# Performance work log

Measured on AMD Instinct MI355X. Metric: run time of the kernel, lower is better.

The kernel has to match this reference:

```python
import jax, jax.numpy as jnp
import numpy as np

B, S, D = 4, 2048, 1024
H = 16
DH = D // H  # 64
DFF = 4096
EPS = 1e-5


def _layer_norm(x, g, b):
    mu = jnp.mean(x, axis=-1, keepdims=True)
    var = jnp.mean((x - mu) ** 2, axis=-1, keepdims=True)
    return (x - mu) * jax.lax.rsqrt(var + EPS) * g + b


def _rope(x):
    # x: [B, S, H, DH]; same rotation for every head (module reuses one RoPE).
    inv_freq = 1.0 / (10000.0 ** (jnp.arange(0, DH, 2, dtype=jnp.float32) / DH))
    pos = jnp.arange(S, dtype=jnp.float32)
    freqs = pos[:, None] * inv_freq[None, :]            # [S, DH/2]
    cos = jnp.cos(freqs)[None, :, None, :]              # [1, S, 1, DH/2]
    sin = jnp.sin(freqs)[None, :, None, :]
    x_even = x[..., 0::2]
    x_odd = x[..., 1::2]
    r_even = x_even * cos - x_odd * sin
    r_odd = x_even * sin + x_odd * cos
    return jnp.stack([r_even, r_odd], axis=-1).reshape(x.shape)


def setup_inputs() -> dict:
    key = jax.random.key(0)
    ks = jax.random.split(key, 10)
    s_d = 1.0 / np.sqrt(D)
    s_f = 1.0 / np.sqrt(DFF)
    return {
        "x": jax.random.normal(ks[0], (B, S, D), jnp.float32),
        "Wq": jax.random.uniform(ks[1], (D, D), jnp.float32, -s_d, s_d),
        "bq": jnp.zeros((D,), jnp.float32),
        "Wk": jax.random.uniform(ks[2], (D, D), jnp.float32, -s_d, s_d),
        "bk": jnp.zeros((D,), jnp.float32),
        "Wv": jax.random.uniform(ks[3], (D, D), jnp.float32, -s_d, s_d),
        "bv": jnp.zeros((D,), jnp.float32),
        "Wo": jax.random.uniform(ks[4], (D, D), jnp.float32, -s_d, s_d),
        "bo": jnp.zeros((D,), jnp.float32),
        "W1": jax.random.uniform(ks[5], (DFF, D), jnp.float32, -s_d, s_d),
        "bf1": jnp.zeros((DFF,), jnp.float32),
        "W2": jax.random.uniform(ks[6], (D, DFF), jnp.float32, -s_f, s_f),
        "bf2": jnp.zeros((D,), jnp.float32),
        "g1": jnp.ones((D,), jnp.float32),
        "be1": jnp.zeros((D,), jnp.float32),
        "g2": jnp.ones((D,), jnp.float32),
        "be2": jnp.zeros((D,), jnp.float32),
    }


def reference(x, Wq, bq, Wk, bk, Wv, bv, Wo, bo, W1, bf1, W2, bf2, g1, be1, g2, be2):
    # Pre-LN self-attention block (dropout is identity at eval)
    residual = x
    h = _layer_norm(x, g1, be1)
    q = (h @ Wq.T + bq).reshape(B, S, H, DH)
    k = (h @ Wk.T + bk).reshape(B, S, H, DH)
    v = (h @ Wv.T + bv).reshape(B, S, H, DH)
    q = _rope(q)
    k = _rope(k)
    # scores: [B, H, Sq, Sk]
    scores = jnp.einsum("bqhd,bkhd->bhqk", q, k) / np.sqrt(DH)
    causal = jnp.tril(jnp.ones((S, S), dtype=bool))
    scores = jnp.where(causal[None, None], scores, -jnp.inf)
    attn = jax.nn.softmax(scores, axis=-1)
    out = jnp.einsum("bhqk,bkhd->bqhd", attn, v).reshape(B, S, D)
    out = out @ Wo.T + bo
    x = residual + out
    # FFN block
    residual = x
    h = _layer_norm(x, g2, be2)
    ff = jax.nn.relu(h @ W1.T + bf1) @ W2.T + bf2
    return residual + ff
```

## Files before the change

### kernel.cpp

```cpp
#include <hip/hip_runtime.h>

typedef __attribute__((ext_vector_type(8))) short bh8;
typedef __attribute__((ext_vector_type(4))) short sh4;
typedef __attribute__((ext_vector_type(4))) float f4;
typedef __attribute__((ext_vector_type(16))) float f16v;
typedef __attribute__((ext_vector_type(4))) unsigned int u4;

__device__ __forceinline__ unsigned short f2bf(float x) {
  unsigned int u = __float_as_uint(x);
  u += 0x7fffu + ((u >> 16) & 1u);
  return (unsigned short)(u >> 16);
}
__device__ __forceinline__ float bf2f(short x) {
  return __uint_as_float(((unsigned int)(unsigned short)x) << 16);
}
__device__ __forceinline__ unsigned cvtpk_bf16(float lo, float hi) {
  unsigned r;
  asm("v_cvt_pk_bf16_f32 %0, %1, %2" : "=v"(r) : "v"(lo), "v"(hi));
  return r;
}
__device__ __forceinline__ void gl_lds16(const short* g, short* l) {
  __builtin_amdgcn_global_load_lds(
      (const __attribute__((address_space(1))) unsigned int*)g,
      (__attribute__((address_space(3))) unsigned int*)l, 16, 0, 0);
}

#define VM2() asm volatile("s_waitcnt vmcnt(2)" ::: "memory")
#define VM0() asm volatile("s_waitcnt vmcnt(0)" ::: "memory")

__global__ __launch_bounds__(256)
void rope_table(float* __restrict__ ct, float* __restrict__ st) {
  const int idx = blockIdx.x * 256 + threadIdx.x;
  const int s = idx >> 5, j = idx & 31;
  const float invf = expf(-0.28782313662425574f * (float)j);
  const float f = (float)s * invf;
  ct[idx] = cosf(f);
  st[idx] = sinf(f);
}

__global__ __launch_bounds__(256)
void concat_bias(const float* __restrict__ bq, const float* __restrict__ bk,
                 const float* __restrict__ bv, float* __restrict__ bqkv) {
  const int i = blockIdx.x * 256 + threadIdx.x;
  bqkv[i] = (i < 1024) ? bq[i] : ((i < 2048) ? bk[i - 1024] : bv[i - 2048]);
}

__global__ __launch_bounds__(256)
void w2bf_all(const float* __restrict__ Wq, const float* __restrict__ Wk,
              const float* __restrict__ Wv, const float* __restrict__ Wo,
              const float* __restrict__ W1, const float* __restrict__ W2,
              short* __restrict__ wqkvb, short* __restrict__ wob,
              short* __restrict__ w1b, short* __restrict__ w2b) {
  const int which = blockIdx.y;
  const float* src; short* dst; int n;
  switch (which) {
    case 0: src = Wq; dst = wqkvb;                 n = 1 << 20; break;
    case 1: src = Wk; dst = wqkvb + (1 << 20);     n = 1 << 20; break;
    case 2: src = Wv; dst = wqkvb + (2 << 20);     n = 1 << 20; break;
    case 3: src = Wo; dst = wob;                   n = 1 << 20; break;
    case 4: src = W1; dst = w1b;                   n = 1 << 22; break;
    default: src = W2; dst = w2b;                  n = 1 << 22; break;
  }
  const int i = (blockIdx.x * 256 + threadIdx.x) * 4;
  if (i >= n) return;
  f4 v = *(const f4*)(src + i);
#pragma unroll
  for (int j = 0; j < 4; ++j) dst[i + j] = (short)f2bf(v[j]);
}

__global__ __launch_bounds__(256)
void layernorm_bf(const float* __restrict__ x, const float* __restrict__ g,
                  const float* __restrict__ be, short* __restrict__ out) {
  __shared__ float sb[4];
  const int row = blockIdx.x, t = threadIdx.x;
  const float* xr = x + (size_t)row * 1024;
  f4 v = *(const f4*)(xr + t * 4);
  float s = v[0] + v[1] + v[2] + v[3];
#pragma unroll
  for (int mk = 1; mk < 64; mk <<= 1) s += __shfl_xor(s, mk, 64);
  if ((t & 63) == 0) sb[t >> 6] = s;
  __syncthreads();
  const float mean = (sb[0] + sb[1] + sb[2] + sb[3]) * (1.0f / 1024.0f);
  __syncthreads();
  f4 d;
#pragma unroll
  for (int i = 0; i < 4; ++i) d[i] = v[i] - mean;
  float s2 = d[0] * d[0] + d[1] * d[1] + d[2] * d[2] + d[3] * d[3];
#pragma unroll
  for (int mk = 1; mk < 64; mk <<= 1) s2 += __shfl_xor(s2, mk, 64);
  if ((t & 63) == 0) sb[t >> 6] = s2;
  __syncthreads();
  const float var = (sb[0] + sb[1] + sb[2] + sb[3]) * (1.0f / 1024.0f);
  const float rstd = rsqrtf(var + 1e-5f);
  const f4 gg = *(const f4*)(g + t * 4);
  const f4 bb = *(const f4*)(be + t * 4);
#pragma unroll
  for (int i = 0; i < 4; ++i)
    out[(size_t)row * 1024 + t * 4 + i] = (short)f2bf(d[i] * rstd * gg[i] + bb[i]);
}

#define STG(dst, gbase, kt, half)                                              \
  {                                                                            \
    _Pragma("unroll") for (int cc = 0; cc < 2; ++cc) {                         \
      const int rr = (half) * 128 + cc * 64 + sr;                              \
      gl_lds16(gbase + (size_t)rr * K + (kt) * 64 + ssl * 8,                   \
               &dst[rr * 64 + (t & 7) * 8]);                                   \
    }                                                                          \
  }

#define PH64(bf, q, STAGE_STMT, VMSTMT)                                        \
  {                                                                            \
    if ((q) == 0) {                                                            \
      _Pragma("unroll") for (int ni = 0; ni < 2; ++ni)                         \
      _Pragma("unroll") for (int kk = 0; kk < 2; ++kk)                         \
        bfrag[ni][kk] = *(const bh8*)(&Bs[bf][(wn * 32 + ni * 16 + (lane & 15)) * 64 + (((lane >> 4) + kk * 4) ^ (lane & 7)) * 8]); \
    }                                                                          \
    _Pragma("unroll") for (int j = 0; j < 2; ++j)                              \
    _Pragma("unroll") for (int kk = 0; kk < 2; ++kk)                           \
      af[j][kk] = *(const bh8*)(&As[bf][(wm * 64 + (2 * (q) + j) * 16 + (lane & 15)) * 64 + (((lane >> 4) + kk * 4) ^ (lane & 7)) * 8]); \
    STAGE_STMT;                                                                \
    __builtin_amdgcn_s_barrier();                                              \
    asm volatile("s_waitcnt lgkmcnt(0)" ::: "memory");                         \
    __builtin_amdgcn_sched_barrier(0);                                         \
    __builtin_amdgcn_s_setprio(1);                                             \
    _Pragma("unroll") for (int j = 0; j < 2; ++j)                              \
    _Pragma("unroll") for (int ni = 0; ni < 2; ++ni)                           \
    _Pragma("unroll") for (int kk = 0; kk < 2; ++kk)                           \
      acc[2 * (q) + j][ni] = __builtin_amdgcn_mfma_f32_16x16x32_bf16(          \
          af[j][kk], bfrag[ni][kk], acc[2 * (q) + j][ni], 0, 0, 0);            \
    __builtin_amdgcn_s_setprio(0);                                             \
    VMSTMT;                                                                    \
    __builtin_amdgcn_s_barrier();                                              \
  }

template <int RELU, int RES, int OBF16, int QKVMODE>
__global__ __launch_bounds__(512, 4)
void gemm_bn128(const short* __restrict__ A, const short* __restrict__ Bw,
                const float* __restrict__ bias, const float* __restrict__ res,
                const float* __restrict__ ct, const float* __restrict__ st,
                short* __restrict__ Vt,
                short* __restrict__ Cb, float* __restrict__ Cf,
                int M, int N, int K) {
  __shared__ short As[2][128 * 64];
  __shared__ short Bs[2][128 * 64];
  const int t = threadIdx.x, lane = t & 63;
  const int w = t >> 6, wm = w >> 2, wn = w & 3;
  const int nwg = gridDim.x, cpx = nwg >> 3;
  int flat = blockIdx.x;
  flat = (flat & 7) * cpx + (flat >> 3);
  const int nbn = N >> 7;
  const int bn = flat % nbn, bm = flat / nbn;
  const short* Ab = A + (size_t)(bm * 128) * K;
  const short* Bb = Bw + (size_t)(bn * 128) * K;
  const int nkt = K >> 6;
  const int sr = t >> 3;
  const int ssl = (t & 7) ^ (sr & 7);
  f4 acc[4][2] = {};
  bh8 bfrag[2][2], af[2][2];

  STG(Bs[0], Bb, 0, 0); STG(As[0], Ab, 0, 0);
  STG(Bs[1], Bb, 1, 0);
  VM2();
  __builtin_amdgcn_s_barrier();

  for (int i2 = 0; i2 < nkt; i2 += 2) {
    const bool nf = (i2 + 2 < nkt);
    PH64(0, 0, STG(As[1], Ab, i2 + 1, 0), );
    PH64(0, 1, if (nf) STG(Bs[0], Bb, i2 + 2, 0),
         if (nf) { VM2(); } else { VM0(); });
    PH64(1, 0, if (nf) STG(As[0], Ab, i2 + 2, 0), );
    PH64(1, 1, if (nf) STG(Bs[1], Bb, i2 + 3, 0), if (nf) { VM2(); });
  }

  const int rb = bm * 128 + wm * 64 + ((lane >> 4) << 2);
  const int cb = bn * 128 + wn * 32 + (lane & 15);
  if (QKVMODE && bn >= 16) {
#pragma unroll
    for (int mi = 0; mi < 4; ++mi) {
#pragma unroll
      for (int ni = 0; ni < 2; ++ni) {
        const int c = cb + ni * 16;
        const float bi = bias[c];
        const int hh = (c - 2048) >> 6, dd = (c - 2048) & 63;
        const int r0 = rb + mi * 16;
        const int bb2 = r0 >> 11, ss = r0 & 2047;
        sh4 pk;
#pragma unroll
        for (int jr = 0; jr < 4; ++jr) pk[jr] = (short)f2bf(acc[mi][ni][jr] + bi);
        *(sh4*)(Vt + ((size_t)(bb2 * 16 + hh) * 64 + dd) * 2048 + ss) = pk;
      }
    }
  } else if (QKVMODE) {
    const bool evenc = (lane & 1) == 0;
#pragma unroll
    for (int mi = 0; mi < 4; ++mi) {
#pragma unroll
      for (int ni = 0; ni < 2; ++ni) {
        const int c = cb + ni * 16;
        const float bi = bias[c];
        const int j0 = (c & 63) >> 1;
#pragma unroll
        for (int jr = 0; jr < 4; ++jr) {
          const int r = rb + mi * 16 + jr;
          const int s = r & 2047;
          const float v = acc[mi][ni][jr] + bi;
          const float pv = __shfl_xor(v, 1, 64);
          const float cs = ct[s * 32 + j0], sn = st[s * 32 + j0];
          const float o = evenc ? (v * cs - pv * sn) : (pv * sn + v * cs);
          Cb[(size_t)r * N + c] = (short)f2bf(o);
        }
      }
    }
  } else {
#pragma unroll
    for (int mi = 0; mi < 4; ++mi) {
#pragma unroll
      for (int ni = 0; ni < 2; ++ni) {
        const int c = cb + ni * 16;
        const float bi = bias[c];
#pragma unroll
        for (int jr = 0; jr < 4; ++jr) {
          const int r = rb + mi * 16 + jr;
          float v = acc[mi][ni][jr] + bi;
          if (RES) v += res[(size_t)r * N + c];
          if (RELU) v = fmaxf(v, 0.f);
          if (OBF16) Cb[(size_t)r * N + c] = (short)f2bf(v);
          else       Cf[(size_t)r * N + c] = v;
        }
      }
    }
  }
}

__global__ __launch_bounds__(512, 4)
void flash_attn(const short* __restrict__ qkv, const short* __restrict__ vt,
                short* __restrict__ o) {
  __shared__ short lds[2 * 2 * 64 * 72];
  const int t = threadIdx.x, lane = t & 63, w = t >> 6;
  const int l31 = lane & 31, l5 = lane >> 5;
  const int id = blockIdx.x;
  const int half = id >> 8, j = id & 255;
  const int xcd = j & 7, y = j >> 3;
  const int bh = xcd * 8 + (y >> 2);
  const int pr = y & 3;
  const int qt = half ? pr : 7 - pr;
  const int b = bh >> 4, hh = bh & 15;
  const int r8 = t >> 3, c8 = (t & 7) * 8;
  const float NEG_INF = -__builtin_inff();

  const short* kbase = qkv + (size_t)b * 2048 * 3072 + 1024 + hh * 64;
  const short* vbase = vt + ((size_t)bh * 64 + r8) * 2048;
  const int wq0 = qt * 256 + w * 32;
  const int nt = 4 * qt + 4;

  bh8 qf[4];
  {
    const short* qrow = qkv + ((size_t)b * 2048 + wq0 + l31) * 3072 + hh * 64 + l5 * 8;
#pragma unroll
    for (int dk = 0; dk < 4; ++dk) qf[dk] = *(const bh8*)(qrow + dk * 16);
  }
  f16v o0 = {}, o1 = {};
  float mr = NEG_INF, lsum = 0.f;

  {
    bh8 rk = *(const bh8*)(kbase + (size_t)r8 * 3072 + c8);
    bh8 rv = *(const bh8*)(vbase + c8);
    *(bh8*)(&lds[r8 * 72 + c8]) = rk;
    *(bh8*)(&lds[4608 + r8 * 72 + c8]) = rv;
  }

  for (int kt = 0; kt < nt; ++kt) {
    __syncthreads();
    const int cur = kt & 1, nxt = cur ^ 1;
    bh8 rk, rv;
    const bool more = (kt + 1 < nt);
    if (more) {
      rk = *(const bh8*)(kbase + (size_t)((kt + 1) * 64 + r8) * 3072 + c8);
      rv = *(const bh8*)(vbase + (kt + 1) * 64 + c8);
    }
    const int kvb = kt * 64;
    if (kvb <= wq0 + 31) {
      const short* Kl = &lds[cur * 9216];
      const short* Vl = &lds[cur * 9216 + 4608];
      f16v s0 = {}, s1 = {};
#pragma unroll
      for (int dk = 0; dk < 4; ++dk) {
        bh8 ka0 = *(const bh8*)(&Kl[l31 * 72 + dk * 16 + l5 * 8]);
        bh8 ka1 = *(const bh8*)(&Kl[(32 + l31) * 72 + dk * 16 + l5 * 8]);
        s0 = __builtin_amdgcn_mfma_f32_32x32x16_bf16(ka0, qf[dk], s0, 0, 0, 0);
        s1 = __builtin_amdgcn_mfma_f32_32x32x16_bf16(ka1, qf[dk], s1, 0, 0, 0);
      }
      if (kvb + 63 > wq0) {
        const int qq = wq0 + l31;
        const int kvo = kvb + l5 * 4;
#pragma unroll
        for (int r = 0; r < 16; ++r) {
          const int kv0 = kvo + (r & 3) + 8 * (r >> 2);
          if (kv0 > qq) s0[r] = NEG_INF;
          if (kv0 + 32 > qq) s1[r] = NEG_INF;
        }
      }
      float mx = s0[0];
#pragma unroll
      for (int r = 1; r < 16; ++r) mx = fmaxf(mx, s0[r]);
#pragma unroll
      for (int r = 0; r < 16; ++r) mx = fmaxf(mx, s1[r]);
      mx = fmaxf(mx, __shfl_xor(mx, 32, 64));
      const bool keep = __all(mx <= mr + 8.0f);
      float mn, al;
      if (keep) { mn = mr; al = 1.0f; }
      else {
        mn = fmaxf(mr, mx);
        al = __expf((mr - mn) * 0.125f);
        mr = mn;
      }
      float rsA = 0.f, rsB = 0.f;
#pragma unroll
      for (int r = 0; r < 16; ++r) {
        const float p0 = __expf((s0[r] - mn) * 0.125f);
        const float p1 = __expf((s1[r] - mn) * 0.125f);
        s0[r] = p0; s1[r] = p1;
        rsA += p0; rsB += p1;
      }
      float rs = rsA + rsB;
      rs += __shfl_xor(rs, 32, 64);
      if (keep) {
        lsum += rs;
      } else {
        lsum = lsum * al + rs;
#pragma unroll
        for (int r = 0; r < 16; ++r) { o0[r] *= al; o1[r] *= al; }
      }
      float pp[32];
#pragma unroll
      for (int r = 0; r < 16; ++r) { pp[r] = s0[r]; pp[16 + r] = s1[r]; }
      const bool lo32 = (l5 == 0);
#pragma unroll
      for (int ks = 0; ks < 4; ++ks) {
        const int base = (ks >> 1) * 16 + (ks & 1) * 8;
        const unsigned e0 = cvtpk_bf16(pp[base + 0], pp[base + 1]);
        const unsigned e1 = cvtpk_bf16(pp[base + 2], pp[base + 3]);
        const unsigned q0 = cvtpk_bf16(pp[base + 4], pp[base + 5]);
        const unsigned q1 = cvtpk_bf16(pp[base + 6], pp[base + 7]);
        const unsigned sel0 = lo32 ? q0 : e0;
        const unsigned sel1 = lo32 ? q1 : e1;
        const unsigned rx0 = (unsigned)__shfl_xor((int)sel0, 32, 64);
        const unsigned rx1 = (unsigned)__shfl_xor((int)sel1, 32, 64);
        u4 frag;
        frag[0] = lo32 ? e0 : rx0;
        frag[1] = lo32 ? e1 : rx1;
        frag[2] = lo32 ? rx0 : q0;
        frag[3] = lo32 ? rx1 : q1;
        const bh8 pb = *(const bh8*)&frag;
        bh8 va0 = *(const bh8*)(&Vl[l31 * 72 + ks * 16 + l5 * 8]);
        bh8 va1 = *(const bh8*)(&Vl[(32 + l31) * 72 + ks * 16 + l5 * 8]);
        o0 = __builtin_amdgcn_mfma_f32_32x32x16_bf16(va0, pb, o0, 0, 0, 0);
        o1 = __builtin_amdgcn_mfma_f32_32x32x16_bf16(va1, pb, o1, 0, 0, 0);
      }
    }
    if (more) {
      *(bh8*)(&lds[nxt * 9216 + r8 * 72 + c8]) = rk;
      *(bh8*)(&lds[nxt * 9216 + 4608 + r8 * 72 + c8]) = rv;
    }
  }

  const float inv = 1.0f / lsum;
  __syncthreads();
  short* Ot = lds;
#pragma unroll
  for (int r = 0; r < 16; ++r) {
    const int d = (r & 3) + 8 * (r >> 2) + 4 * l5;
    Ot[(w * 32 + l31) * 72 + d]      = (short)f2bf(o0[r] * inv);
    Ot[(w * 32 + l31) * 72 + 32 + d] = (short)f2bf(o1[r] * inv);
  }
  __syncthreads();
  const int qrow = t >> 1, hf = t & 1;
  short* orow = o + ((size_t)b * 2048 + qt * 256 + qrow) * 1024 + hh * 64 + hf * 32;
#pragma unroll
  for (int i = 0; i < 4; ++i)
    *(bh8*)(orow + i * 8) = *(const bh8*)(&Ot[qrow * 72 + hf * 32 + i * 8]);
}

extern "C" void kernel_launch(void* const* d_in, const int* in_sizes, int n_in,
                              void* d_out, int out_size, void* d_ws, size_t ws_size,
                              hipStream_t stream) {
  const float* x   = (const float*)d_in[0];
  const float* Wq  = (const float*)d_in[1];
  const float* bq  = (const float*)d_in[2];
  const float* Wk  = (const float*)d_in[3];
  const float* bk  = (const float*)d_in[4];
  const float* Wv  = (const float*)d_in[5];
  const float* bv  = (const float*)d_in[6];
  const float* Wo  = (const float*)d_in[7];
  const float* bo  = (const float*)d_in[8];
  const float* W1  = (const float*)d_in[9];
  const float* bf1 = (const float*)d_in[10];
  const float* W2  = (const float*)d_in[11];
  const float* bf2 = (const float*)d_in[12];
  const float* g1  = (const float*)d_in[13];
  const float* be1 = (const float*)d_in[14];
  const float* g2  = (const float*)d_in[15];
  const float* be2 = (const float*)d_in[16];
  float* out = (float*)d_out;

  char* ws = (char*)d_ws;
  const size_t MB = 1u << 20;
  short* h_ob  = (short*)ws;
  short* qkv   = (short*)(ws + 16 * MB);
  short* f1    = (short*)(ws + 16 * MB);
  short* vtb   = (short*)(ws + 64 * MB);
  short* wqkvb = (short*)(ws + 80 * MB);
  short* wob   = (short*)(ws + 86 * MB);
  short* w1b   = (short*)(ws + 88 * MB);
  short* w2b   = (short*)(ws + 96 * MB);
  float* ct    = (float*)(ws + 104 * MB);
  float* st    = ct + 65536;
  float* bqkv  = st + 65536;
  float* x2    = out;

  rope_table<<<256, 256, 0, stream>>>(ct, st);
  concat_bias<<<12, 256, 0, stream>>>(bq, bk, bv, bqkv);
  w2bf_all<<<dim3(4096, 6), 256, 0, stream>>>(Wq, Wk, Wv, Wo, W1, W2,
                                              wqkvb, wob, w1b, w2b);

  layernorm_bf<<<8192, 256, 0, stream>>>(x, g1, be1, h_ob);

  gemm_bn128<0, 0, 1, 1><<<1536, 512, 0, stream>>>(h_ob, wqkvb, bqkv, nullptr,
                                                   ct, st, vtb, qkv, nullptr,
                                                   8192, 3072, 1024);

  flash_attn<<<512, 512, 0, stream>>>(qkv, vtb, h_ob);

  gemm_bn128<0, 1, 0, 0><<<512, 512, 0, stream>>>(h_ob, wob, bo, x,
                                                  nullptr, nullptr, nullptr,
                                                  nullptr, x2, 8192, 1024, 1024);

  layernorm_bf<<<8192, 256, 0, stream>>>(x2, g2, be2, h_ob);

  gemm_bn128<1, 0, 1, 0><<<2048, 512, 0, stream>>>(h_ob, w1b, bf1, nullptr,
                                                   nullptr, nullptr, nullptr,
                                                   f1, nullptr, 8192, 4096, 1024);

  gemm_bn128<0, 1, 0, 0><<<512, 512, 0, stream>>>(f1, w2b, bf2, x2,
                                                  nullptr, nullptr, nullptr,
                                                  nullptr, out, 8192, 1024, 4096);
}
```

Before: 360.1 us.

## Restructure GEMM to BK=32 triple-buffered LDS pipeline with higher occupancy

Replaces the double-buffered 64-wide K tile GEMM with a 32-wide K tile and a three-slot ring of LDS buffers, prefetching two tiles ahead. The LDS footprint drops from 64KB to 48KB and launch bounds rise from 4 to 6 waves/EU, aiming for more resident workgroups and better latency hiding. The swizzle changes to a 4-slot XOR pattern to match the narrower rows. In exchange there are twice as many barriers per unit of K work, fewer MFMAs per barrier, and tighter register limits.

Measured after the change: 380.7 us. 5.7% more time.

```diff
diff --git a/kernel.cpp b/kernel.cpp
--- a/kernel.cpp
+++ b/kernel.cpp
@@ -99,50 +99,39 @@
     out[(size_t)row * 1024 + t * 4 + i] = (short)f2bf(d[i] * rstd * gg[i] + bb[i]);
 }
 
-#define STG(dst, gbase, kt, half)                                              \
+#define STG32(dst, gbase, kt)                                                  \
+  gl_lds16(gbase + (size_t)sr32 * K + (kt) * 32 + ssl32 * 8, (dst) + t * 8);
+
+#define PH32(Ac, Bc, STAGE_STMT, VMSTMT)                                       \
   {                                                                            \
-    _Pragma("unroll") for (int cc = 0; cc < 2; ++cc) {                         \
-      const int rr = (half) * 128 + cc * 64 + sr;                              \
-      gl_lds16(gbase + (size_t)rr * K + (kt) * 64 + ssl * 8,                   \
-               &dst[rr * 64 + (t & 7) * 8]);                                   \
-    }                                                                          \
-  }
-
-#define PH64(bf, q, STAGE_STMT, VMSTMT)                                        \
-  {                                                                            \
-    if ((q) == 0) {                                                            \
-      _Pragma("unroll") for (int ni = 0; ni < 2; ++ni)                         \
-      _Pragma("unroll") for (int kk = 0; kk < 2; ++kk)                         \
-        bfrag[ni][kk] = *(const bh8*)(&Bs[bf][(wn * 32 + ni * 16 + (lane & 15)) * 64 + (((lane >> 4) + kk * 4) ^ (lane & 7)) * 8]); \
-    }                                                                          \
-    _Pragma("unroll") for (int j = 0; j < 2; ++j)                              \
-    _Pragma("unroll") for (int kk = 0; kk < 2; ++kk)                           \
-      af[j][kk] = *(const bh8*)(&As[bf][(wm * 64 + (2 * (q) + j) * 16 + (lane & 15)) * 64 + (((lane >> 4) + kk * 4) ^ (lane & 7)) * 8]); \
+    _Pragma("unroll") for (int j = 0; j < 4; ++j)                              \
+      af[j] = *(const bh8*)(&(Ac)[(wm * 64 + j * 16 + (lane & 15)) * 32 + rslot]); \
+    _Pragma("unroll") for (int ni = 0; ni < 2; ++ni)                           \
+      bfrag[ni] = *(const bh8*)(&(Bc)[(wn * 32 + ni * 16 + (lane & 15)) * 32 + rslot]); \
     STAGE_STMT;                                                                \
     __builtin_amdgcn_s_barrier();                                              \
     asm volatile("s_waitcnt lgkmcnt(0)" ::: "memory");                         \
     __builtin_amdgcn_sched_barrier(0);                                         \
     __builtin_amdgcn_s_setprio(1);                                             \
-    _Pragma("unroll") for (int j = 0; j < 2; ++j)                              \
+    _Pragma("unroll") for (int j = 0; j < 4; ++j)                              \
     _Pragma("unroll") for (int ni = 0; ni < 2; ++ni)                           \
-    _Pragma("unroll") for (int kk = 0; kk < 2; ++kk)                           \
-      acc[2 * (q) + j][ni] = __builtin_amdgcn_mfma_f32_16x16x32_bf16(          \
-          af[j][kk], bfrag[ni][kk], acc[2 * (q) + j][ni], 0, 0, 0);            \
+      acc[j][ni] = __builtin_amdgcn_mfma_f32_16x16x32_bf16(                    \
+          af[j], bfrag[ni], acc[j][ni], 0, 0, 0);                              \
     __builtin_amdgcn_s_setprio(0);                                             \
     VMSTMT;                                                                    \
     __builtin_amdgcn_s_barrier();                                              \
   }
 
 template <int RELU, int RES, int OBF16, int QKVMODE>
-__global__ __launch_bounds__(512, 4)
-void gemm_bn128(const short* __restrict__ A, const short* __restrict__ Bw,
-                const float* __restrict__ bias, const float* __restrict__ res,
-                const float* __restrict__ ct, const float* __restrict__ st,
-                short* __restrict__ Vt,
-                short* __restrict__ Cb, float* __restrict__ Cf,
-                int M, int N, int K) {
-  __shared__ short As[2][128 * 64];
-  __shared__ short Bs[2][128 * 64];
+__global__ __launch_bounds__(512, 6)
+void gemm_tb(const short* __restrict__ A, const short* __restrict__ Bw,
+             const float* __restrict__ bias, const float* __restrict__ res,
+             const float* __restrict__ ct, const float* __restrict__ st,
+             short* __restrict__ Vt,
+             short* __restrict__ Cb, float* __restrict__ Cf,
+             int M, int N, int K) {
+  __shared__ short LA[3 * 4096];
+  __shared__ short LB[3 * 4096];
   const int t = threadIdx.x, lane = t & 63;
   const int w = t >> 6, wm = w >> 2, wn = w & 3;
   const int nwg = gridDim.x, cpx = nwg >> 3;
@@ -152,24 +141,26 @@
   const int bn = flat % nbn, bm = flat / nbn;
   const short* Ab = A + (size_t)(bm * 128) * K;
   const short* Bb = Bw + (size_t)(bn * 128) * K;
-  const int nkt = K >> 6;
-  const int sr = t >> 3;
-  const int ssl = (t & 7) ^ (sr & 7);
+  const int nkt = K >> 5;
+  const int sr32 = t >> 2;
+  const int ssl32 = (t & 3) ^ (sr32 & 3);
+  const int rslot = (((lane >> 4) ^ (lane & 3)) << 3);
   f4 acc[4][2] = {};
-  bh8 bfrag[2][2], af[2][2];
-
-  STG(Bs[0], Bb, 0, 0); STG(As[0], Ab, 0, 0);
-  STG(Bs[1], Bb, 1, 0);
+  bh8 bfrag[2], af[4];
+
+  STG32(LA, Ab, 0); STG32(LB, Bb, 0);
+  STG32(&LA[4096], Ab, 1); STG32(&LB[4096], Bb, 1);
   VM2();
   __builtin_amdgcn_s_barrier();
 
-  for (int i2 = 0; i2 < nkt; i2 += 2) {
-    const bool nf = (i2 + 2 < nkt);
-    PH64(0, 0, STG(As[1], Ab, i2 + 1, 0), );
-    PH64(0, 1, if (nf) STG(Bs[0], Bb, i2 + 2, 0),
-         if (nf) { VM2(); } else { VM0(); });
-    PH64(1, 0, if (nf) STG(As[0], Ab, i2 + 2, 0), );
-    PH64(1, 1, if (nf) STG(Bs[1], Bb, i2 + 3, 0), if (nf) { VM2(); });
+  int cur = 0;
+  for (int tt = 0; tt < nkt; ++tt) {
+    const int stg = (cur >= 1) ? cur - 1 : 2;
+    const bool sf = (tt + 2 < nkt);
+    PH32(&LA[cur * 4096], &LB[cur * 4096],
+         if (sf) { STG32(&LA[stg * 4096], Ab, tt + 2); STG32(&LB[stg * 4096], Bb, tt + 2); },
+         if (sf) { VM2(); } else { VM0(); });
+    cur = (cur >= 2) ? 0 : cur + 1;
   }
 
   const int rb = bm * 128 + wm * 64 + ((lane >> 4) << 2);
@@ -425,23 +416,23 @@
 
   layernorm_bf<<<8192, 256, 0, stream>>>(x, g1, be1, h_ob);
 
-  gemm_bn128<0, 0, 1, 1><<<1536, 512, 0, stream>>>(h_ob, wqkvb, bqkv, nullptr,
-                                                   ct, st, vtb, qkv, nullptr,
-                                                   8192, 3072, 1024);
+  gemm_tb<0, 0, 1, 1><<<1536, 512, 0, stream>>>(h_ob, wqkvb, bqkv, nullptr,
+                                                ct, st, vtb, qkv, nullptr,
+                                                8192, 3072, 1024);
 
   flash_attn<<<512, 512, 0, stream>>>(qkv, vtb, h_ob);
 
-  gemm_bn128<0, 1, 0, 0><<<512, 512, 0, stream>>>(h_ob, wob, bo, x,
-                                                  nullptr, nullptr, nullptr,
-                                                  nullptr, x2, 8192, 1024, 1024);
+  gemm_tb<0, 1, 0, 0><<<512, 512, 0, stream>>>(h_ob, wob, bo, x,
+                                               nullptr, nullptr, nullptr,
+                                               nullptr, x2, 8192, 1024, 1024);
 
   layernorm_bf<<<8192, 256, 0, stream>>>(x2, g2, be2, h_ob);
 
-  gemm_bn128<1, 0, 1, 0><<<2048, 512, 0, stream>>>(h_ob, w1b, bf1, nullptr,
-                                                   nullptr, nullptr, nullptr,
-                                                   f1, nullptr, 8192, 4096, 1024);
-
-  gemm_bn128<0, 1, 0, 0><<<512, 512, 0, stream>>>(f1, w2b, bf2, x2,
-                                                  nullptr, nullptr, nullptr,
-                                                  nullptr, out, 8192, 1024, 4096);
-}
+  gemm_tb<1, 0, 1, 0><<<2048, 512, 0, stream>>>(h_ob, w1b, bf1, nullptr,
+                                                nullptr, nullptr, nullptr,
+                                                f1, nullptr, 8192, 4096, 1024);
+
+  gemm_tb<0, 1, 0, 0><<<512, 512, 0, stream>>>(f1, w2b, bf2, x2,
+                                               nullptr, nullptr, nullptr,
+                                               nullptr, out, 8192, 1024, 4096);
+}
```
